# Kernel tuning notes

Hardware: AMD Instinct MI355X
Metric: run time of the kernel (lower is better)

## Reference

```python
import jax, jax.numpy as jnp
import numpy as np

T_STEPS = 10       # T_pos = T_neg = 10 hardcoded in forward
ATTN_SCALE = 0.125 # scale hardcoded in forward (not head_dim**-0.5)
V_TH = 1.0         # spikingjelly IFNode defaults: v_threshold=1.0, v_reset=0.0 (hard reset)
SG_ALPHA = 4.0     # default Sigmoid surrogate alpha

@jax.custom_vjp
def spike(v):
    return (v >= 0.0).astype(v.dtype)

def _spike_fwd(v):
    return spike(v), v

def _spike_bwd(v, g):
    sg = jax.nn.sigmoid(SG_ALPHA * v)
    return (g * SG_ALPHA * sg * (1.0 - sg),)

spike.defvjp(_spike_fwd, _spike_bwd)

def if_node_const_input(y, T=T_STEPS):
    """Multi-step IF neuron driven by the SAME input y at every step.
    charge: v += y; fire: s = H(v - 1); hard reset: v = (1 - s) * v.
    Returns spikes of shape [T, *y.shape]."""
    def step(v, _):
        v = v + y
        s = spike(v - V_TH)
        v = (1.0 - s) * v
        return v, s
    _, spikes = jax.lax.scan(step, jnp.zeros_like(y), None, length=T)
    return spikes

def setup_inputs() -> dict:
    key = jax.random.key(0)
    ks = jax.random.split(key, 6)
    N, C = 2048, 2048
    x = jax.random.normal(ks[0], (N, C), dtype=jnp.float32)
    freqs_cis = jax.random.normal(ks[1], (N, 64), dtype=jnp.float32)  # unused by forward
    w_scale = 0.02
    wq = jax.random.normal(ks[2], (C, C), dtype=jnp.float32) * w_scale
    wk = jax.random.normal(ks[3], (C, C), dtype=jnp.float32) * w_scale
    wv = jax.random.normal(ks[4], (C, C), dtype=jnp.float32) * w_scale
    wo = jax.random.normal(ks[5], (C, C), dtype=jnp.float32) * w_scale
    return {"x": x, "freqs_cis": freqs_cis, "wq": wq, "wk": wk, "wv": wv, "wo": wo}

def reference(x, freqs_cis, wq, wk, wv, wo):
    N, C = x.shape
    n_heads, head_dim = 16, 128  # C == n_heads * head_dim; n_kv_heads == n_heads so repeat_kv is a no-op
    T = T_STEPS

    x_pos = jax.nn.relu(x)
    x_neg = jax.nn.relu(-x)

    # Input is identical at every timestep, so apply the linear once, then run IF over T.
    def branch(xb):
        q = if_node_const_input(xb @ wq)  # [T, N, C] binary spikes
        k = if_node_const_input(xb @ wk)
        v = if_node_const_input(xb @ wv)
        return q, k, v

    qp, kp, vp = branch(x_pos)
    qn, kn, vn = branch(x_neg)
    xq = (qp - qn).reshape(T, N, n_heads, head_dim)
    xk = (kp - kn).reshape(T, N, n_heads, head_dim)
    xv = (vp - vn).reshape(T, N, n_heads, head_dim)

    # no-softmax attention over the HEAD axis, per token: [T,N,H,H]
    attn = jnp.einsum('tnhd,tnmd->tnhm', xq, xk) * ATTN_SCALE
    x_attn = jnp.einsum('tnhm,tnmd->tnhd', attn, xv)          # [T,N,H,Dh]
    x_attn = jnp.swapaxes(x_attn, -1, -2).reshape(T, N, C)    # transpose(-1,-2) then merge

    xo = x_attn @ wo  # [T, N, C]
    return xo.mean(axis=0)
```

## Files before the change

### kernel.cpp

```cpp
#include <hip/hip_runtime.h>
#include <hip/hip_bf16.h>


#define LIST_CAP (512u * 1024u)
#define FLAG_EPS 4e-4f

typedef __attribute__((ext_vector_type(8))) short short8;
typedef __attribute__((ext_vector_type(4))) float floatx4;

__device__ const unsigned d_LUT[16] = {0u, 0x3FFu, 0x2AAu, 0x124u, 0x88u,
                                       0x210u, 0x20u, 0x40u, 0x80u, 0x100u,
                                       0x200u, 0u, 0u, 0u, 0u, 0u};

__device__ __forceinline__ void bf16x2_rne(float a, unsigned& p1, unsigned& p2) {
  const unsigned u = __float_as_uint(a);
  const unsigned t1 = u + 0x7FFFu + ((u >> 16) & 1u);
  p1 = t1 >> 16;
  const float r = a - __uint_as_float(t1 & 0xFFFF0000u);
  const unsigned u2 = __float_as_uint(r);
  p2 = (u2 + 0x7FFFu + ((u2 >> 16) & 1u)) >> 16;
}

template <int ZERO_CNT>
__global__ __launch_bounds__(256) void wsplit(
    const float* __restrict__ W0, const float* __restrict__ W1,
    const float* __restrict__ W2, unsigned short* __restrict__ Bpk,
    int NCT, unsigned* __restrict__ cnt) {
  if (ZERO_CNT && blockIdx.x == 0 && blockIdx.y == 0 && threadIdx.x == 0)
    *cnt = 0u;
  __shared__ float Wf[32 * 132];
  const int ct = blockIdx.x, k0 = blockIdx.y * 32;
  const int c0 = ct * 128;
  const int sel = c0 >> 11;
  const float* W = (sel == 0) ? W0 : ((sel == 1) ? W1 : W2);
  const int cc0 = c0 & 2047;
  const int t = threadIdx.x;

  const int kr = t >> 3, cq = (t & 7) * 16;
#pragma unroll
  for (int u = 0; u < 4; u++) {
    const float4 v = *(const float4*)(W + (size_t)(k0 + kr) * 2048 + cc0 + cq + 4 * u);
    *(float4*)&Wf[kr * 132 + cq + 4 * u] = v;
  }
  __syncthreads();

  const int cc = t >> 1, ch0 = (t & 1) * 2;
  unsigned short* img1 = Bpk + ((size_t)(0 * NCT + ct) * 64 + blockIdx.y) * 4096;
  unsigned short* img2 = Bpk + ((size_t)(1 * NCT + ct) * 64 + blockIdx.y) * 4096;
#pragma unroll
  for (int c = ch0; c < ch0 + 2; c++) {
    unsigned q1[8], q2[8];
#pragma unroll
    for (int e = 0; e < 8; e++) bf16x2_rne(Wf[(c * 8 + e) * 132 + cc], q1[e], q2[e]);
    const int off = cc * 32 + 8 * (c ^ ((cc >> 1) & 3));
    uint4 P1, P2;
    P1.x = q1[0] | (q1[1] << 16); P1.y = q1[2] | (q1[3] << 16);
    P1.z = q1[4] | (q1[5] << 16); P1.w = q1[6] | (q1[7] << 16);
    P2.x = q2[0] | (q2[1] << 16); P2.y = q2[2] | (q2[3] << 16);
    P2.z = q2[4] | (q2[5] << 16); P2.w = q2[6] | (q2[7] << 16);
    *(uint4*)&img1[off] = P1;
    *(uint4*)&img2[off] = P2;
  }
}

template <int RELU>
__global__ __launch_bounds__(256) void asplit(
    const float* __restrict__ src, unsigned short* __restrict__ Apk, int NRT) {
  const int rt = blockIdx.x, k0i = blockIdx.y;
  const int t = threadIdx.x;
  const int r = t >> 1, half = t & 1;
  int grow = rt * 128 + r;
  float sgn = 1.f;
  if (RELU && grow >= 2048) { grow -= 2048; sgn = -1.f; }
  const float* s = src + (size_t)grow * 2048 + k0i * 32 + half * 16;
  float f[16];
#pragma unroll
  for (int u = 0; u < 4; u++) {
    const float4 v = *(const float4*)(s + 4 * u);
    f[4 * u + 0] = v.x; f[4 * u + 1] = v.y;
    f[4 * u + 2] = v.z; f[4 * u + 3] = v.w;
  }
  if (RELU) {
#pragma unroll
    for (int e = 0; e < 16; e++) f[e] = fmaxf(sgn * f[e], 0.f);
  }
  unsigned q1[16], q2[16];
#pragma unroll
  for (int e = 0; e < 16; e++) bf16x2_rne(f[e], q1[e], q2[e]);

  unsigned short* img1 = Apk + ((size_t)(0 * NRT + rt) * 64 + k0i) * 4096;
  unsigned short* img2 = Apk + ((size_t)(1 * NRT + rt) * 64 + k0i) * 4096;
#pragma unroll
  for (int cc = 0; cc < 2; cc++) {
    const int c = half * 2 + cc;
    const int off = r * 32 + 8 * (c ^ ((r >> 1) & 3));
    const int e0 = cc * 8;
    uint4 P1, P2;
    P1.x = q1[e0 + 0] | (q1[e0 + 1] << 16); P1.y = q1[e0 + 2] | (q1[e0 + 3] << 16);
    P1.z = q1[e0 + 4] | (q1[e0 + 5] << 16); P1.w = q1[e0 + 6] | (q1[e0 + 7] << 16);
    P2.x = q2[e0 + 0] | (q2[e0 + 1] << 16); P2.y = q2[e0 + 2] | (q2[e0 + 3] << 16);
    P2.z = q2[e0 + 4] | (q2[e0 + 5] << 16); P2.w = q2[e0 + 6] | (q2[e0 + 7] << 16);
    *(uint4*)&img1[off] = P1;
    *(uint4*)&img2[off] = P2;
  }
}

template <int MODE>
__global__ __launch_bounds__(256) void gemm_dma(
    const unsigned short* __restrict__ Apk, const unsigned short* __restrict__ Bpk,
    int NRT, int NCT, unsigned char* __restrict__ MaskJ,
    unsigned* __restrict__ list, unsigned* __restrict__ cnt,
    float* __restrict__ Out) {
  __shared__ unsigned short sh[4][4096];

  const int tid = threadIdx.x;
  const int bx = blockIdx.x, by = blockIdx.y;
  const int lane = tid & 63, wave = tid >> 6;
  const int wr = wave >> 1, wc = wave & 1;
  const int lm = lane & 15, lg = lane >> 4;

  const unsigned short* gsrc =
      (wave < 2) ? (Apk + ((size_t)(wave * NRT + by) * 64) * 4096)
                 : (Bpk + ((size_t)((wave - 2) * NCT + bx) * 64) * 4096);

  floatx4 acc[4][4];
#pragma unroll
  for (int i = 0; i < 4; i++)
#pragma unroll
    for (int j = 0; j < 4; j++) acc[i][j] = (floatx4){0.f, 0.f, 0.f, 0.f};

  for (int k0i = 0; k0i < 64; k0i++) {
    __syncthreads();
    const unsigned short* gp = gsrc + (size_t)k0i * 4096;
#pragma unroll
    for (int i = 0; i < 8; i++) {
      __builtin_amdgcn_global_load_lds(
          (const __attribute__((address_space(1))) unsigned*)(gp + i * 512 + lane * 8),
          (__attribute__((address_space(3))) unsigned*)(&sh[wave][i * 512]), 16, 0, 0);
    }
    __syncthreads();

    short8 a1[4], a2[4], b1[4], b2[4];
#pragma unroll
    for (int i = 0; i < 4; i++) {
      const int row = 64 * wr + 16 * i + lm;
      const int off = row * 32 + 8 * (lg ^ ((row >> 1) & 3));
      a1[i] = *(const short8*)&sh[0][off];
      a2[i] = *(const short8*)&sh[1][off];
    }
#pragma unroll
    for (int j = 0; j < 4; j++) {
      const int row = 64 * wc + 16 * j + lm;
      const int off = row * 32 + 8 * (lg ^ ((row >> 1) & 3));
      b1[j] = *(const short8*)&sh[2][off];
      b2[j] = *(const short8*)&sh[3][off];
    }
#pragma unroll
    for (int i = 0; i < 4; i++)
#pragma unroll
      for (int j = 0; j < 4; j++)
        acc[i][j] = __builtin_amdgcn_mfma_f32_16x16x32_bf16(a1[i], b1[j], acc[i][j], 0, 0, 0);
#pragma unroll
    for (int i = 0; i < 4; i++)
#pragma unroll
      for (int j = 0; j < 4; j++)
        acc[i][j] = __builtin_amdgcn_mfma_f32_16x16x32_bf16(a1[i], b2[j], acc[i][j], 0, 0, 0);
#pragma unroll
    for (int i = 0; i < 4; i++)
#pragma unroll
      for (int j = 0; j < 4; j++)
        acc[i][j] = __builtin_amdgcn_mfma_f32_16x16x32_bf16(a2[i], b1[j], acc[i][j], 0, 0, 0);
  }

#pragma unroll
  for (int i = 0; i < 4; i++) {
#pragma unroll
    for (int j = 0; j < 4; j++) {
      const int gn = bx * 128 + 64 * wc + 16 * j + lm;
#pragma unroll
      for (int vv = 0; vv < 4; vv++) {
        const int gm = by * 128 + 64 * wr + 16 * i + 4 * lg + vv;
        const float y = acc[i][j][vv];
        if (MODE == 1) {
          Out[(size_t)gm * 2048 + gn] = y * 0.1f;
        } else {
          float r = __builtin_amdgcn_rcpf(y);
          r = fminf(fmaxf(r, -1.0f), 12.0f);
          const float jf = floorf(r);
          const float d0 = fmaf(jf, y, -1.0f);
          const float i0 = fminf(fmaxf(jf, 1.0f), 10.0f);
          const float i1 = fminf(fmaxf(jf + 1.0f, 1.0f), 10.0f);
          const float e0 = fmaf(i0, y, -1.0f);
          const float e1 = fmaf(i1, y, -1.0f);
          const float mind = fminf(fabsf(e0), fabsf(e1));
          const unsigned J = (unsigned)(int)((d0 >= 0.0f) ? jf : jf + 1.0f);
          MaskJ[(size_t)gm * 6144 + gn] = (unsigned char)((J <= 10u) ? J : 0u);
          if (mind < FLAG_EPS) {
            const unsigned idx = atomicAdd(cnt, 1u);
            if (idx < LIST_CAP) list[idx] = ((unsigned)gm << 13) | (unsigned)gn;
          }
        }
      }
    }
  }
}

__global__ __launch_bounds__(256) void transpose_w(
    const float* __restrict__ W0, const float* __restrict__ W1,
    const float* __restrict__ W2, float* __restrict__ WT) {
  __shared__ float tile[32][33];
  const int k0 = blockIdx.x * 32;
  const int c0 = blockIdx.y * 32;
  const int sel = c0 >> 11;
  const float* W = (sel == 0) ? W0 : ((sel == 1) ? W1 : W2);
  const int cc0 = c0 & 2047;
  const int tx = threadIdx.x, ty = threadIdx.y;
#pragma unroll
  for (int rep = 0; rep < 4; rep++)
    tile[ty + 8 * rep][tx] = W[(size_t)(k0 + ty + 8 * rep) * 2048 + cc0 + tx];
  __syncthreads();
#pragma unroll
  for (int rep = 0; rep < 4; rep++)
    WT[(size_t)(c0 + ty + 8 * rep) * 2048 + k0 + tx] = tile[tx][ty + 8 * rep];
}

__global__ __launch_bounds__(256) void rescue(
    const float* __restrict__ X, const float* __restrict__ WT,
    const unsigned* __restrict__ list, const unsigned* __restrict__ cnt,
    unsigned char* __restrict__ MaskJ) {
  const unsigned nItems = min(*cnt, LIST_CAP);
  const unsigned gtid = blockIdx.x * blockDim.x + threadIdx.x;
  const unsigned wave = gtid >> 6, lane = gtid & 63;
  const unsigned nWaves = (gridDim.x * blockDim.x) >> 6;

  for (unsigned i = wave; i < nItems; i += nWaves) {
    const unsigned e = list[i];
    const int r = (int)(e >> 13), c = (int)(e & 8191u);
    const float* xrow = X + (size_t)((r < 2048) ? r : r - 2048) * 2048;
    const float sg = (r < 2048) ? 1.f : -1.f;
    const float* wrow = WT + (size_t)c * 2048;
    double s = 0.0;
#pragma unroll
    for (int it = 0; it < 8; it++) {
      const int k = (it * 64 + (int)lane) * 4;
      const float4 xv = *(const float4*)(xrow + k);
      const float4 wv = *(const float4*)(wrow + k);
      const float a0 = fmaxf(sg * xv.x, 0.f);
      const float a1 = fmaxf(sg * xv.y, 0.f);
      const float a2 = fmaxf(sg * xv.z, 0.f);
      const float a3 = fmaxf(sg * xv.w, 0.f);
      s += (double)a0 * (double)wv.x + (double)a1 * (double)wv.y +
           (double)a2 * (double)wv.z + (double)a3 * (double)wv.w;
    }
#pragma unroll
    for (int off = 32; off > 0; off >>= 1) s += __shfl_down(s, off);
    if (lane == 0) {
      double v = 0.0;
      unsigned J = 0;
#pragma unroll
      for (int t = 0; t < 10; t++) {
        v += s;
        if (J == 0u && v >= 1.0) J = (unsigned)(t + 1);
      }
      MaskJ[(size_t)r * 6144 + c] = (unsigned char)J;
    }
  }
}

__global__ __launch_bounds__(256) void spike_attn(const unsigned char* __restrict__ MaskJ,
                                                  float* __restrict__ xbar) {
  const int n = blockIdx.x;
  const int tid = threadIdx.x;

  __shared__ float xqT[128 * 17];
  __shared__ float xkT[128 * 17];
  __shared__ float xvT[128 * 17];
  __shared__ float attnS[16 * 17];
  __shared__ unsigned lutS[16];

  if (tid < 16) lutS[tid] = d_LUT[tid];
  __syncthreads();

  const unsigned char* mp = MaskJ + (size_t)n * 6144;
  const unsigned char* mn = MaskJ + (size_t)(n + 2048) * 6144;

  unsigned q_p[8], q_n[8], k_p[8], k_n[8], v_p[8], v_n[8];
#pragma unroll
  for (int j = 0; j < 8; j++) {
    const int c = tid + 256 * j;
    q_p[j] = lutS[mp[c]];        q_n[j] = lutS[mn[c]];
    k_p[j] = lutS[mp[2048 + c]]; k_n[j] = lutS[mn[2048 + c]];
    v_p[j] = lutS[mp[4096 + c]]; v_n[j] = lutS[mn[4096 + c]];
  }

  float acc[8];
#pragma unroll
  for (int j = 0; j < 8; j++) acc[j] = 0.f;

  for (int t = 0; t < 10; t++) {
#pragma unroll
    for (int j = 0; j < 8; j++) {
      const int c = tid + 256 * j;
      const int d = c & 127, h = c >> 7;
      const int a = d * 17 + h;
      xqT[a] = (float)((q_p[j] >> t) & 1u) - (float)((q_n[j] >> t) & 1u);
      xkT[a] = (float)((k_p[j] >> t) & 1u) - (float)((k_n[j] >> t) & 1u);
      xvT[a] = (float)((v_p[j] >> t) & 1u) - (float)((v_n[j] >> t) & 1u);
    }
    __syncthreads();

    {
      const int h = tid >> 4, m = tid & 15;
      float a = 0.f;
#pragma unroll
      for (int d = 0; d < 128; d++) a += xqT[d * 17 + h] * xkT[d * 17 + m];
      attnS[h * 17 + m] = a * 0.125f;
    }
    __syncthreads();

#pragma unroll
    for (int j = 0; j < 8; j++) {
      const int o = tid + 256 * j;
      const int h = o & 15, d = o >> 4;
      float s = 0.f;
#pragma unroll
      for (int m = 0; m < 16; m++) s += attnS[h * 17 + m] * xvT[d * 17 + m];
      acc[j] += s;
    }
    __syncthreads();
  }

#pragma unroll
  for (int j = 0; j < 8; j++) xbar[(size_t)n * 2048 + tid + 256 * j] = acc[j];
}

extern "C" void kernel_launch(void* const* d_in, const int* in_sizes, int n_in,
                              void* d_out, int out_size, void* d_ws, size_t ws_size,
                              hipStream_t stream) {
  const float* x = (const float*)d_in[0];
  const float* wq = (const float*)d_in[2];
  const float* wk = (const float*)d_in[3];
  const float* wv = (const float*)d_in[4];
  const float* wo = (const float*)d_in[5];
  float* out = (float*)d_out;

  char* ws = (char*)d_ws;
  unsigned char* MaskJ = (unsigned char*)ws;
  unsigned short* WOpk = (unsigned short*)ws;
  char* reg2 = ws + (size_t)4096 * 6144;
  unsigned short* Bpk = (unsigned short*)reg2;
  float* WT = (float*)reg2;
  unsigned short* Xbpk = (unsigned short*)reg2;
  char* reg3 = reg2 + (size_t)6144 * 2048 * 2 * 2;
  unsigned short* Apk = (unsigned short*)reg3;
  float* xbar = (float*)reg3;
  unsigned* list = (unsigned*)(reg3 + (size_t)4096 * 2048 * 2 * 2);
  unsigned* cnt = list + LIST_CAP;

  wsplit<1><<<dim3(48, 64), 256, 0, stream>>>(wq, wk, wv, Bpk, 48, cnt);
  asplit<1><<<dim3(32, 64), 256, 0, stream>>>(x, Apk, 32);
  gemm_dma<0><<<dim3(48, 32), 256, 0, stream>>>(Apk, Bpk, 32, 48, MaskJ, list, cnt, nullptr);
  transpose_w<<<dim3(64, 192), dim3(32, 8), 0, stream>>>(wq, wk, wv, WT);
  rescue<<<2048, 256, 0, stream>>>(x, WT, list, cnt, MaskJ);
  spike_attn<<<2048, 256, 0, stream>>>(MaskJ, xbar);
  wsplit<0><<<dim3(16, 64), 256, 0, stream>>>(wo, wo, wo, WOpk, 16, nullptr);
  asplit<0><<<dim3(16, 64), 256, 0, stream>>>(xbar, Xbpk, 16);
  gemm_dma<1><<<dim3(16, 16), 256, 0, stream>>>(Xbpk, WOpk, 16, 16, nullptr, nullptr, nullptr, out);
}
```

Measured before the change: 932.9 us.

## Double-buffer GEMM LDS loads and use ballot/popcount spike attention

The GEMM kernel now double-buffers its shared-memory tiles, so the DMA for the next K-slice is issued before the current slice is consumed, and one barrier per iteration is dropped. This overlaps global-to-LDS transfer with MFMA work but doubles LDS use, which can lower occupancy. The spike attention kernel packs q/k spikes into 64-bit ballot masks and computes the head-by-head dot products with popcounts instead of 128-term float loops. It also relays out the V tile and caches attention rows in registers. An unused LUT load is added to the GEMM.

```diff
diff --git a/kernel.cpp b/kernel.cpp
--- a/kernel.cpp
+++ b/kernel.cpp
@@ -111,7 +111,8 @@
     int NRT, int NCT, unsigned char* __restrict__ MaskJ,
     unsigned* __restrict__ list, unsigned* __restrict__ cnt,
     float* __restrict__ Out) {
-  __shared__ unsigned short sh[4][4096];
+  __shared__ unsigned short sh[2][4][4096];
+  __shared__ unsigned lutS[16];
 
   const int tid = threadIdx.x;
   const int bx = blockIdx.x, by = blockIdx.y;
@@ -119,41 +120,49 @@
   const int wr = wave >> 1, wc = wave & 1;
   const int lm = lane & 15, lg = lane >> 4;
 
+  if (MODE == 0 && tid < 16) lutS[tid] = d_LUT[tid];
+
   const unsigned short* gsrc =
       (wave < 2) ? (Apk + ((size_t)(wave * NRT + by) * 64) * 4096)
                  : (Bpk + ((size_t)((wave - 2) * NCT + bx) * 64) * 4096);
 
+  auto dma8 = [&](unsigned short* dst, const unsigned short* src) {
+#pragma unroll
+    for (int i = 0; i < 8; i++) {
+      __builtin_amdgcn_global_load_lds(
+          (const __attribute__((address_space(1))) unsigned*)(src + i * 512 + lane * 8),
+          (__attribute__((address_space(3))) unsigned*)(dst + i * 512), 16, 0, 0);
+    }
+  };
+
   floatx4 acc[4][4];
 #pragma unroll
   for (int i = 0; i < 4; i++)
 #pragma unroll
     for (int j = 0; j < 4; j++) acc[i][j] = (floatx4){0.f, 0.f, 0.f, 0.f};
+
+  dma8(&sh[0][wave][0], gsrc);
 
   for (int k0i = 0; k0i < 64; k0i++) {
     __syncthreads();
-    const unsigned short* gp = gsrc + (size_t)k0i * 4096;
-#pragma unroll
-    for (int i = 0; i < 8; i++) {
-      __builtin_amdgcn_global_load_lds(
-          (const __attribute__((address_space(1))) unsigned*)(gp + i * 512 + lane * 8),
-          (__attribute__((address_space(3))) unsigned*)(&sh[wave][i * 512]), 16, 0, 0);
-    }
-    __syncthreads();
-
+    if (k0i + 1 < 64)
+      dma8(&sh[(k0i + 1) & 1][wave][0], gsrc + (size_t)(k0i + 1) * 4096);
+
+    const unsigned short(*cur)[4096] = sh[k0i & 1];
     short8 a1[4], a2[4], b1[4], b2[4];
 #pragma unroll
     for (int i = 0; i < 4; i++) {
       const int row = 64 * wr + 16 * i + lm;
       const int off = row * 32 + 8 * (lg ^ ((row >> 1) & 3));
-      a1[i] = *(const short8*)&sh[0][off];
-      a2[i] = *(const short8*)&sh[1][off];
+      a1[i] = *(const short8*)&cur[0][off];
+      a2[i] = *(const short8*)&cur[1][off];
     }
 #pragma unroll
     for (int j = 0; j < 4; j++) {
       const int row = 64 * wc + 16 * j + lm;
       const int off = row * 32 + 8 * (lg ^ ((row >> 1) & 3));
-      b1[j] = *(const short8*)&sh[2][off];
-      b2[j] = *(const short8*)&sh[3][off];
+      b1[j] = *(const short8*)&cur[2][off];
+      b2[j] = *(const short8*)&cur[3][off];
     }
 #pragma unroll
     for (int i = 0; i < 4; i++)
@@ -271,10 +280,10 @@
                                                   float* __restrict__ xbar) {
   const int n = blockIdx.x;
   const int tid = threadIdx.x;
-
-  __shared__ float xqT[128 * 17];
-  __shared__ float xkT[128 * 17];
-  __shared__ float xvT[128 * 17];
+  const int lane = tid & 63;
+
+  __shared__ unsigned long long qpB[16][2], qnB[16][2], kpB[16][2], knB[16][2];
+  __shared__ float xvT[16 * 132];
   __shared__ float attnS[16 * 17];
   __shared__ unsigned lutS[16];
 
@@ -301,31 +310,48 @@
 #pragma unroll
     for (int j = 0; j < 8; j++) {
       const int c = tid + 256 * j;
-      const int d = c & 127, h = c >> 7;
-      const int a = d * 17 + h;
-      xqT[a] = (float)((q_p[j] >> t) & 1u) - (float)((q_n[j] >> t) & 1u);
-      xkT[a] = (float)((k_p[j] >> t) & 1u) - (float)((k_n[j] >> t) & 1u);
-      xvT[a] = (float)((v_p[j] >> t) & 1u) - (float)((v_n[j] >> t) & 1u);
+      const unsigned long long bqp = __ballot((q_p[j] >> t) & 1u);
+      const unsigned long long bqn = __ballot((q_n[j] >> t) & 1u);
+      const unsigned long long bkp = __ballot((k_p[j] >> t) & 1u);
+      const unsigned long long bkn = __ballot((k_n[j] >> t) & 1u);
+      const int h = c >> 7, word = (c >> 6) & 1;
+      if (lane == 0) {
+        qpB[h][word] = bqp; qnB[h][word] = bqn;
+        kpB[h][word] = bkp; knB[h][word] = bkn;
+      }
+      const int m = h, d = c & 127;
+      xvT[m * 132 + d] =
+          (float)((v_p[j] >> t) & 1u) - (float)((v_n[j] >> t) & 1u);
     }
     __syncthreads();
 
     {
       const int h = tid >> 4, m = tid & 15;
-      float a = 0.f;
-#pragma unroll
-      for (int d = 0; d < 128; d++) a += xqT[d * 17 + h] * xkT[d * 17 + m];
-      attnS[h * 17 + m] = a * 0.125f;
+      int dot = 0;
+#pragma unroll
+      for (int w = 0; w < 2; w++) {
+        const unsigned long long qp = qpB[h][w], qn = qnB[h][w];
+        const unsigned long long kp = kpB[m][w], kn = knB[m][w];
+        dot += __popcll(qp & kp) + __popcll(qn & kn) -
+               __popcll(qp & kn) - __popcll(qn & kp);
+      }
+      attnS[h * 17 + m] = (float)dot * 0.125f;
     }
     __syncthreads();
 
-#pragma unroll
-    for (int j = 0; j < 8; j++) {
-      const int o = tid + 256 * j;
-      const int h = o & 15, d = o >> 4;
-      float s = 0.f;
-#pragma unroll
-      for (int m = 0; m < 16; m++) s += attnS[h * 17 + m] * xvT[d * 17 + m];
-      acc[j] += s;
+    {
+      const int h = tid & 15;
+      float arow[16];
+#pragma unroll
+      for (int m = 0; m < 16; m++) arow[m] = attnS[h * 17 + m];
+#pragma unroll
+      for (int j = 0; j < 8; j++) {
+        const int d = (tid + 256 * j) >> 4;
+        float s = 0.f;
+#pragma unroll
+        for (int m = 0; m < 16; m++) s += arow[m] * xvT[m * 132 + d];
+        acc[j] += s;
+      }
     }
     __syncthreads();
   }
```

Result: faster. 838.6 us (-10.1%).
